# Kernel optimization log

Hardware: AMD Instinct MI355X
Metric: run time of the kernel (lower is better)

## Reference

```python
import jax, jax.numpy as jnp
import numpy as np

N_NODES = 50000
N_EDGES = 800000
D_IN = 128
D_OUT = 128


def setup_inputs() -> dict:
    key = jax.random.key(0)
    k1, k2, k3, k4, k5, k6 = jax.random.split(key, 6)
    curr_fea = jax.random.normal(k1, (N_NODES, D_IN), dtype=jnp.float32)
    edge_index = jax.random.randint(k2, (2, N_EDGES), 0, N_NODES, dtype=jnp.int64)
    s = 1.0 / np.sqrt(D_IN)
    W_self = jax.random.uniform(k3, (D_OUT, D_IN), jnp.float32, -s, s)
    b_self = jax.random.uniform(k4, (D_OUT,), jnp.float32, -s, s)
    W_neig = jax.random.uniform(k5, (D_OUT, D_IN), jnp.float32, -s, s)
    b_neig = jax.random.uniform(k6, (D_OUT,), jnp.float32, -s, s)
    return {"curr_fea": curr_fea, "edge_index": edge_index,
            "W_self": W_self, "b_self": b_self,
            "W_neig": W_neig, "b_neig": b_neig}


def reference(curr_fea, edge_index, W_self, b_self, W_neig, b_neig):
    num_nodes = curr_fea.shape[0]
    src, dst = edge_index[0], edge_index[1]
    # symmetrize: messages flow both directions
    src_all = jnp.concatenate([src, dst], axis=0)  # [2E]
    dst_all = jnp.concatenate([dst, src], axis=0)  # [2E]
    # gather neighbor features then scatter-add into destination nodes
    nei_sum = jax.ops.segment_sum(curr_fea[src_all], dst_all,
                                  num_segments=num_nodes)  # [N, d]
    out = (curr_fea @ W_self.T + b_self) + (nei_sum @ W_neig.T + b_neig)
    return out
```

## Files before the change

kernel.cpp:

```cpp
#include <hip/hip_runtime.h>

#define DD 128
#define BM 64
#define BK 32
#define BKN 64
#define NBMAX 1024
#define ECH 2048
#define CAP 2304
#define PADC 136

typedef __attribute__((ext_vector_type(8))) short bf16x8;
typedef __attribute__((ext_vector_type(4))) float f32x4;

__device__ __forceinline__ unsigned short f2b(float x) {
    unsigned u = __float_as_uint(x);
    u += 0x7fffu + ((u >> 16) & 1u);
    return (unsigned short)(u >> 16);
}
__device__ __forceinline__ float b2f_lo(unsigned v) { return __uint_as_float(v << 16); }
__device__ __forceinline__ float b2f_hi(unsigned v) { return __uint_as_float(v & 0xffff0000u); }
__device__ __forceinline__ float bf(unsigned short u) {
    return __uint_as_float((unsigned)u << 16);
}

__device__ __forceinline__ int detect_rf(const void* ei_raw, int E, int lane) {
    const unsigned long long* p = (const unsigned long long*)ei_raw;
    int n64 = E < 64 ? E : 64;
    bool big = (lane < n64) && (p[lane] >= (1ULL << 32));
    return (__ballot(big) == 0ULL) ? 1 : 0;
}

__global__ void detect_kernel(const unsigned long long* __restrict__ ei,
                              int n64, int* __restrict__ flag) {
    int i = threadIdx.x;
    bool big = (i < n64) && (ei[i] >= (1ULL << 32));
    unsigned long long b = __ballot(big);
    if (i == 0) *flag = (b == 0ULL) ? 1 : 0;
}

__global__ void cvt_all_kernel(const float* __restrict__ fea,
                               const float* __restrict__ Ws,
                               const float* __restrict__ Wn,
                               unsigned short* __restrict__ feaB,
                               unsigned short* __restrict__ Wcat, int n4) {
    int i = blockIdx.x * 256 + threadIdx.x;
    if (i < n4) {
        float4 v = reinterpret_cast<const float4*>(fea)[i];
        ushort4 o;
        o.x = f2b(v.x); o.y = f2b(v.y); o.z = f2b(v.z); o.w = f2b(v.w);
        reinterpret_cast<ushort4*>(feaB)[i] = o;
    } else if (i < n4 + 2 * DD * DD / 4) {
        int k4 = i - n4;
        int n = k4 >> 6;
        int kk = (k4 & 63) * 4;
        float4 v = (kk < DD) ? *reinterpret_cast<const float4*>(Ws + n * DD + kk)
                             : *reinterpret_cast<const float4*>(Wn + n * DD + kk - DD);
        ushort4 o;
        o.x = f2b(v.x); o.y = f2b(v.y); o.z = f2b(v.z); o.w = f2b(v.w);
        reinterpret_cast<ushort4*>(Wcat)[k4] = o;
    }
}

__global__ void cvt_fea_kernel(const float* __restrict__ in,
                               unsigned short* __restrict__ out, int n4) {
    int i = blockIdx.x * 256 + threadIdx.x;
    if (i >= n4) return;
    float4 v = reinterpret_cast<const float4*>(in)[i];
    ushort4 o;
    o.x = f2b(v.x); o.y = f2b(v.y); o.z = f2b(v.z); o.w = f2b(v.w);
    reinterpret_cast<ushort4*>(out)[i] = o;
}

__global__ void cvt_w_kernel(const float* __restrict__ Ws,
                             const float* __restrict__ Wn,
                             unsigned short* __restrict__ Wcat) {
    int i = blockIdx.x * 256 + threadIdx.x;
    int n = i >> 8, k = i & 255;
    float v = (k < DD) ? Ws[n * DD + k] : Wn[n * DD + (k - DD)];
    Wcat[i] = f2b(v);
}

__launch_bounds__(512)
__global__ void bin_kernel(const void* __restrict__ ei_raw, int E,
                           unsigned* __restrict__ region,
                           unsigned* __restrict__ gcur, int nbk) {
    __shared__ unsigned stage[2 * ECH];
    __shared__ unsigned cnt[NBMAX];
    __shared__ unsigned start[NBMAX];
    __shared__ unsigned cursor[NBMAX];
    __shared__ unsigned gbase[NBMAX];
    __shared__ unsigned scanT[512];

    const int t = threadIdx.x;
    const int lane = t & 63;
    const int rf = detect_rf(ei_raw, E, lane);

    for (int b = t; b < NBMAX; b += 512) { cnt[b] = 0; cursor[b] = 0; }
    __syncthreads();

    const int e0 = blockIdx.x * ECH;
    int es[4], ed[4];
#pragma unroll
    for (int j = 0; j < 4; ++j) {
        int e = e0 + j * 512 + t;
        if (e < E) {
            if (rf) {
                const long long* p = (const long long*)ei_raw;
                es[j] = (int)p[e]; ed[j] = (int)p[e + E];
            } else {
                const int* p = (const int*)ei_raw;
                es[j] = p[e]; ed[j] = p[e + E];
            }
            atomicAdd(&cnt[ed[j] >> 6], 1u);
            atomicAdd(&cnt[es[j] >> 6], 1u);
        } else {
            es[j] = -1; ed[j] = -1;
        }
    }
    __syncthreads();

    unsigned lv[2]; unsigned lsum = 0;
#pragma unroll
    for (int j = 0; j < 2; ++j) { lv[j] = cnt[t * 2 + j]; lsum += lv[j]; }
    scanT[t] = lsum; __syncthreads();
    for (int o = 1; o < 512; o <<= 1) {
        unsigned x = (t >= o) ? scanT[t - o] : 0;
        __syncthreads();
        scanT[t] += x;
        __syncthreads();
    }
    unsigned run = scanT[t] - lsum;
#pragma unroll
    for (int j = 0; j < 2; ++j) { start[t * 2 + j] = run; run += lv[j]; }
    __syncthreads();

#pragma unroll
    for (int j = 0; j < 4; ++j) {
        if (es[j] >= 0) {
            int s = es[j], d = ed[j];
            unsigned p0 = atomicAdd(&cursor[d >> 6], 1u);
            stage[start[d >> 6] + p0] = (unsigned)(d & 63) | ((unsigned)s << 6);
            unsigned p1 = atomicAdd(&cursor[s >> 6], 1u);
            stage[start[s >> 6] + p1] = (unsigned)(s & 63) | ((unsigned)d << 6);
        }
    }
    __syncthreads();

    for (int b = t; b < nbk; b += 512) {
        unsigned c = cnt[b];
        gbase[b] = c ? atomicAdd(&gcur[b], c) : 0;
    }
    __syncthreads();

    const int w = t >> 6;
    for (int b = w; b < nbk; b += 8) {
        unsigned c = cnt[b];
        if (!c) continue;
        unsigned gb = gbase[b], st = start[b];
        for (unsigned l2 = lane; l2 < c; l2 += 64) {
            unsigned idx = gb + l2;
            if (idx < CAP)
                region[(size_t)b * CAP + idx] = stage[st + l2];
        }
    }
}

__launch_bounds__(512)
__global__ void gather_gemm_kernel(const unsigned short* __restrict__ feaB,
                                   const unsigned short* __restrict__ Wcat,
                                   const unsigned* __restrict__ region,
                                   const unsigned* __restrict__ gcur,
                                   const float* __restrict__ bs,
                                   const float* __restrict__ bn,
                                   float* __restrict__ out, int M) {
    __shared__ unsigned srt[CAP];
    __shared__ unsigned short neiL[BKN][PADC];
    __shared__ unsigned c64[BKN];
    __shared__ unsigned p64[BKN + 1];
    __shared__ unsigned cur64[BKN];

    const int t = threadIdx.x, b = blockIdx.x;
    unsigned cnt = gcur[b];
    if (cnt > CAP) cnt = CAP;
    const unsigned* reg = region + (size_t)b * CAP;

    unsigned ent[5];
#pragma unroll
    for (int q = 0; q < 5; ++q) {
        unsigned i = (unsigned)t + (unsigned)q * 512u;
        ent[q] = (i < cnt) ? reg[i] : 0xFFFFFFFFu;
    }

    if (t < BKN) { c64[t] = 0; cur64[t] = 0; }
    __syncthreads();

#pragma unroll
    for (int q = 0; q < 5; ++q)
        if (ent[q] != 0xFFFFFFFFu) atomicAdd(&c64[ent[q] & 63u], 1u);
    __syncthreads();

    if (t == 0) {
        unsigned r = 0;
        for (int n = 0; n < BKN; ++n) { p64[n] = r; r += c64[n]; }
        p64[BKN] = r;
    }
    __syncthreads();

#pragma unroll
    for (int q = 0; q < 5; ++q) {
        if (ent[q] != 0xFFFFFFFFu) {
            unsigned e = ent[q];
            unsigned p = atomicAdd(&cur64[e & 63u], 1u);
            srt[p64[e & 63u] + p] = e >> 6;
        }
    }
    __syncthreads();

    const int w = t >> 6, lane = t & 63;
    const int half = lane >> 5, li = lane & 31;
    const unsigned short* bp = feaB + li * 4;

    for (int n = w; n < BKN; n += 8) {
        int g = b * BKN + n;
        unsigned p = p64[n];
        unsigned d = (g < M) ? c64[n] : 0;
        float a0 = 0.f, a1 = 0.f, a2 = 0.f, a3 = 0.f;
        unsigned j = 0;
        for (; j + 16 <= d; j += 16) {
            ushort4 v[8];
#pragma unroll
            for (int q = 0; q < 8; ++q) {
                unsigned s = srt[p + j + 2 * q + half];
                v[q] = *reinterpret_cast<const ushort4*>(bp + (size_t)s * DD);
            }
#pragma unroll
            for (int q = 0; q < 8; ++q) {
                a0 += bf(v[q].x); a1 += bf(v[q].y);
                a2 += bf(v[q].z); a3 += bf(v[q].w);
            }
        }
        for (; j + 2 <= d; j += 2) {
            unsigned s = srt[p + j + half];
            ushort4 v = *reinterpret_cast<const ushort4*>(bp + (size_t)s * DD);
            a0 += bf(v.x); a1 += bf(v.y); a2 += bf(v.z); a3 += bf(v.w);
        }
        if (j < d && half == 0) {
            unsigned s = srt[p + j];
            ushort4 v = *reinterpret_cast<const ushort4*>(bp + (size_t)s * DD);
            a0 += bf(v.x); a1 += bf(v.y); a2 += bf(v.z); a3 += bf(v.w);
        }
        a0 += __shfl_xor(a0, 32);
        a1 += __shfl_xor(a1, 32);
        a2 += __shfl_xor(a2, 32);
        a3 += __shfl_xor(a3, 32);
        if (half == 0) {
            ushort4 o;
            o.x = f2b(a0); o.y = f2b(a1); o.z = f2b(a2); o.w = f2b(a3);
            *reinterpret_cast<ushort4*>(&neiL[n][li * 4]) = o;
        }
    }
    __syncthreads();

    const int lr = lane & 15, ks = lane >> 4;
    const int rg = w & 3, cgr = w >> 2;
    const int row0 = b * BKN + rg * 16;
    const int rowl = rg * 16 + lr;
    const int rowg = row0 + lr;
    const int col0 = cgr * 64;

    f32x4 acc[4] = {};
#pragma unroll
    for (int kb = 0; kb < 256; kb += 32) {
        bf16x8 a;
        if (kb < DD) {
            if (rowg < M)
                a = *reinterpret_cast<const bf16x8*>(
                    feaB + (size_t)rowg * DD + kb + ks * 8);
            else
                a = bf16x8{0, 0, 0, 0, 0, 0, 0, 0};
        } else {
            a = *reinterpret_cast<const bf16x8*>(&neiL[rowl][(kb - DD) + ks * 8]);
        }
#pragma unroll
        for (int ci = 0; ci < 4; ++ci) {
            int nn = col0 + ci * 16 + lr;
            bf16x8 bb = *reinterpret_cast<const bf16x8*>(
                Wcat + (size_t)nn * 256 + kb + ks * 8);
            acc[ci] = __builtin_amdgcn_mfma_f32_16x16x32_bf16(a, bb, acc[ci], 0, 0, 0);
        }
    }

#pragma unroll
    for (int ci = 0; ci < 4; ++ci) {
        int colg = col0 + ci * 16 + lr;
        float bias = bs[colg] + bn[colg];
        int rbase = row0 + ks * 4;
#pragma unroll
        for (int i2 = 0; i2 < 4; ++i2) {
            int r2 = rbase + i2;
            if (r2 < M) out[(size_t)r2 * DD + colg] = acc[ci][i2] + bias;
        }
    }
}

__global__ void transpose_kernel(const float* __restrict__ Ws,
                                 const float* __restrict__ Wn,
                                 float* __restrict__ Wts,
                                 float* __restrict__ Wtn) {
    int idx = blockIdx.x * blockDim.x + threadIdx.x;
    int i = idx & (DD * DD - 1);
    int col = i >> 7;
    int k = i & (DD - 1);
    if (idx < DD * DD)          Wts[k * DD + col] = Ws[i];
    else if (idx < 2 * DD * DD) Wtn[k * DD + col] = Wn[i];
}

__global__ void hist_kernel(const void* __restrict__ ei_raw,
                            int* __restrict__ deg, int E,
                            const int* __restrict__ flag) {
    int e = blockIdx.x * 256 + threadIdx.x;
    if (e >= E) return;
    int s, d;
    if (*flag) {
        const long long* ei = (const long long*)ei_raw;
        s = (int)ei[e]; d = (int)ei[e + E];
    } else {
        const int* ei = (const int*)ei_raw;
        s = ei[e]; d = ei[e + E];
    }
    atomicAdd(&deg[s], 1);
    atomicAdd(&deg[d], 1);
}

__global__ void scan1_kernel(const int* __restrict__ deg, int* __restrict__ off,
                             int* __restrict__ bsum, int N) {
    __shared__ int sd[256];
    int base = blockIdx.x * 1024;
    int t = threadIdx.x;
    int v[4]; int s = 0;
#pragma unroll
    for (int j = 0; j < 4; ++j) {
        int idx = base + t * 4 + j;
        v[j] = (idx < N) ? deg[idx] : 0;
        s += v[j];
    }
    sd[t] = s; __syncthreads();
    for (int o = 1; o < 256; o <<= 1) {
        int x = (t >= o) ? sd[t - o] : 0;
        __syncthreads();
        sd[t] += x;
        __syncthreads();
    }
    int run = sd[t] - s;
    if (t == 255) bsum[blockIdx.x] = sd[255];
#pragma unroll
    for (int j = 0; j < 4; ++j) {
        int idx = base + t * 4 + j;
        if (idx < N) off[idx] = run;
        run += v[j];
    }
}

__global__ void scan2_kernel(int* __restrict__ bsum, int NB,
                             int* __restrict__ total) {
    __shared__ int sd[256];
    int t = threadIdx.x;
    int v = (t < NB) ? bsum[t] : 0;
    sd[t] = v; __syncthreads();
    for (int o = 1; o < 256; o <<= 1) {
        int x = (t >= o) ? sd[t - o] : 0;
        __syncthreads();
        sd[t] += x;
        __syncthreads();
    }
    if (t < NB) bsum[t] = sd[t] - v;
    if (t == 255) *total = sd[255];
}

__global__ void scan3_kernel(int* __restrict__ off, const int* __restrict__ bsum,
                             int N) {
    int i = blockIdx.x * blockDim.x + threadIdx.x;
    if (i < N) off[i] += bsum[i >> 10];
}

__global__ void fill_kernel(const void* __restrict__ ei_raw,
                            const int* __restrict__ off,
                            int* __restrict__ cursor, int* __restrict__ list,
                            int E, const int* __restrict__ flag) {
    int e = blockIdx.x * 256 + threadIdx.x;
    if (e >= E) return;
    int s, d;
    if (*flag) {
        const long long* ei = (const long long*)ei_raw;
        s = (int)ei[e]; d = (int)ei[e + E];
    } else {
        const int* ei = (const int*)ei_raw;
        s = ei[e]; d = ei[e + E];
    }
    int p0 = atomicAdd(&cursor[d], 1); list[off[d] + p0] = s;
    int p1 = atomicAdd(&cursor[s], 1); list[off[s] + p1] = d;
}

__launch_bounds__(256)
__global__ void gather_b_kernel(const unsigned short* __restrict__ feaB,
                                const int* __restrict__ off,
                                const int* __restrict__ list,
                                unsigned short* __restrict__ neiB, int N) {
    int w = (int)((blockIdx.x * 256 + threadIdx.x) >> 6);
    if (w >= N) return;
    int lane = threadIdx.x & 63;
    int start = off[w], end = off[w + 1];
    float ax = 0.f, ay = 0.f;
    const unsigned short* base = feaB + lane * 2;
    int j = start;
    for (; j + 4 <= end; j += 4) {
        int s0 = list[j], s1 = list[j + 1], s2 = list[j + 2], s3 = list[j + 3];
        unsigned a = *reinterpret_cast<const unsigned*>(base + (size_t)s0 * DD);
        unsigned b = *reinterpret_cast<const unsigned*>(base + (size_t)s1 * DD);
        unsigned c = *reinterpret_cast<const unsigned*>(base + (size_t)s2 * DD);
        unsigned d = *reinterpret_cast<const unsigned*>(base + (size_t)s3 * DD);
        ax += b2f_lo(a) + b2f_lo(b) + b2f_lo(c) + b2f_lo(d);
        ay += b2f_hi(a) + b2f_hi(b) + b2f_hi(c) + b2f_hi(d);
    }
    for (; j < end; ++j) {
        unsigned a = *reinterpret_cast<const unsigned*>(base + (size_t)list[j] * DD);
        ax += b2f_lo(a); ay += b2f_hi(a);
    }
    ushort2 o; o.x = f2b(ax); o.y = f2b(ay);
    *reinterpret_cast<ushort2*>(neiB + (size_t)w * DD + lane * 2) = o;
}

__launch_bounds__(256)
__global__ void gather_f32_kernel(const float* __restrict__ fea,
                                  const int* __restrict__ off,
                                  const int* __restrict__ list,
                                  float* __restrict__ nei, int N) {
    int w = (int)((blockIdx.x * 256 + threadIdx.x) >> 6);
    if (w >= N) return;
    int lane = threadIdx.x & 63;
    int start = off[w], end = off[w + 1];
    float2 acc = make_float2(0.f, 0.f);
    const float* base = fea + (size_t)lane * 2;
    int j = start;
    for (; j + 4 <= end; j += 4) {
        int s0 = list[j], s1 = list[j + 1], s2 = list[j + 2], s3 = list[j + 3];
        float2 a = *reinterpret_cast<const float2*>(base + (size_t)s0 * DD);
        float2 b = *reinterpret_cast<const float2*>(base + (size_t)s1 * DD);
        float2 c = *reinterpret_cast<const float2*>(base + (size_t)s2 * DD);
        float2 e = *reinterpret_cast<const float2*>(base + (size_t)s3 * DD);
        acc.x += a.x + b.x + c.x + e.x;
        acc.y += a.y + b.y + c.y + e.y;
    }
    for (; j < end; ++j) {
        float2 a = *reinterpret_cast<const float2*>(base + (size_t)list[j] * DD);
        acc.x += a.x; acc.y += a.y;
    }
    *reinterpret_cast<float2*>(nei + (size_t)w * DD + lane * 2) = acc;
}

__global__ void scatter_kernel(const float* __restrict__ fea,
                               const void* __restrict__ ei_raw,
                               float* __restrict__ nei,
                               int E, const int* __restrict__ flag) {
    long long r = (long long)blockIdx.x * 8 + (threadIdx.x >> 5);
    if (r >= 2LL * E) return;
    int lr = threadIdx.x & 31;
    int i = (int)(r < E ? r : r - E);
    int s, d;
    if (*flag) {
        const long long* ei = (const long long*)ei_raw;
        s = (int)ei[i]; d = (int)ei[i + E];
    } else {
        const int* ei = (const int*)ei_raw;
        s = ei[i]; d = ei[i + E];
    }
    if (r >= E) { int t = s; s = d; d = t; }
    const float4 v = *reinterpret_cast<const float4*>(fea + (size_t)s * DD + lr * 4);
    float* p = nei + (size_t)d * DD + lr * 4;
    unsafeAtomicAdd(p + 0, v.x);
    unsafeAtomicAdd(p + 1, v.y);
    unsafeAtomicAdd(p + 2, v.z);
    unsafeAtomicAdd(p + 3, v.w);
}

__launch_bounds__(256)
__global__ void gemm_mfma_kernel(const unsigned short* __restrict__ feaB,
                                 const unsigned short* __restrict__ neiB,
                                 const unsigned short* __restrict__ Wcat,
                                 const float* __restrict__ bs,
                                 const float* __restrict__ bn,
                                 float* __restrict__ out, int M) {
    const int w  = threadIdx.x >> 6;
    const int l  = threadIdx.x & 63;
    const int lr = l & 15;
    const int ks = l >> 4;
    const int row0 = blockIdx.x * 128 + w * 32;
    const int col0 = blockIdx.y * 64;

    f32x4 acc[2][4] = {};

#pragma unroll
    for (int kb = 0; kb < 256; kb += 32) {
        const unsigned short* A = (kb < DD) ? feaB : neiB;
        const int klocal = (kb < DD) ? kb : kb - DD;
        bf16x8 a[2];
#pragma unroll
        for (int ri = 0; ri < 2; ++ri) {
            int rowg = row0 + ri * 16 + lr;
            if (rowg < M)
                a[ri] = *reinterpret_cast<const bf16x8*>(
                    A + (size_t)rowg * DD + klocal + ks * 8);
            else
                a[ri] = bf16x8{0, 0, 0, 0, 0, 0, 0, 0};
        }
#pragma unroll
        for (int ci = 0; ci < 4; ++ci) {
            int n = col0 + ci * 16 + lr;
            bf16x8 b = *reinterpret_cast<const bf16x8*>(
                Wcat + (size_t)n * 256 + kb + ks * 8);
#pragma unroll
            for (int ri = 0; ri < 2; ++ri)
                acc[ri][ci] = __builtin_amdgcn_mfma_f32_16x16x32_bf16(
                    a[ri], b, acc[ri][ci], 0, 0, 0);
        }
    }

#pragma unroll
    for (int ci = 0; ci < 4; ++ci) {
        int colg = col0 + ci * 16 + lr;
        float bias = bs[colg] + bn[colg];
#pragma unroll
        for (int ri = 0; ri < 2; ++ri) {
            int rbase = row0 + ri * 16 + ks * 4;
#pragma unroll
            for (int i = 0; i < 4; ++i) {
                int rowg = rbase + i;
                if (rowg < M)
                    out[(size_t)rowg * DD + colg] = acc[ri][ci][i] + bias;
            }
        }
    }
}

__launch_bounds__(256)
__global__ void gemm_kernel(const float* __restrict__ fea,
                            const float* __restrict__ nei,
                            const float* __restrict__ Wts,
                            const float* __restrict__ Wtn,
                            const float* __restrict__ bs,
                            const float* __restrict__ bn,
                            float* __restrict__ out, int M) {
    __shared__ float Fs[BM][BK + 4];
    __shared__ float Ns[BM][BK + 4];
    __shared__ float WsT[BK][DD];
    __shared__ float WnT[BK][DD];

    const int t = threadIdx.x;
    const int cg = t & 31;
    const int rg = t >> 5;
    const int row0 = blockIdx.x * BM;

    float4 acc[8];
#pragma unroll
    for (int r = 0; r < 8; ++r) acc[r] = make_float4(0.f, 0.f, 0.f, 0.f);

    for (int kb = 0; kb < DD; kb += BK) {
#pragma unroll
        for (int j = 0; j < 2; ++j) {
            int idx = t + j * 256;
            int row = idx >> 3;
            int seg = idx & 7;
            int grow = row0 + row;
            float4 fv = make_float4(0.f, 0.f, 0.f, 0.f);
            float4 nv = make_float4(0.f, 0.f, 0.f, 0.f);
            if (grow < M) {
                fv = *reinterpret_cast<const float4*>(fea + (size_t)grow * DD + kb + seg * 4);
                nv = *reinterpret_cast<const float4*>(nei + (size_t)grow * DD + kb + seg * 4);
            }
            *reinterpret_cast<float4*>(&Fs[row][seg * 4]) = fv;
            *reinterpret_cast<float4*>(&Ns[row][seg * 4]) = nv;
        }
#pragma unroll
        for (int j = 0; j < 4; ++j) {
            int idx = t + j * 256;
            int kk = idx >> 5;
            int seg = idx & 31;
            *reinterpret_cast<float4*>(&WsT[kk][seg * 4]) =
                *reinterpret_cast<const float4*>(Wts + (size_t)(kb + kk) * DD + seg * 4);
            *reinterpret_cast<float4*>(&WnT[kk][seg * 4]) =
                *reinterpret_cast<const float4*>(Wtn + (size_t)(kb + kk) * DD + seg * 4);
        }
        __syncthreads();

#pragma unroll
        for (int kk = 0; kk < BK; ++kk) {
            float4 wsv = *reinterpret_cast<const float4*>(&WsT[kk][cg * 4]);
            float4 wnv = *reinterpret_cast<const float4*>(&WnT[kk][cg * 4]);
#pragma unroll
            for (int r = 0; r < 8; ++r) {
                float a = Fs[rg * 8 + r][kk];
                float b = Ns[rg * 8 + r][kk];
                acc[r].x += a * wsv.x + b * wnv.x;
                acc[r].y += a * wsv.y + b * wnv.y;
                acc[r].z += a * wsv.z + b * wnv.z;
                acc[r].w += a * wsv.w + b * wnv.w;
            }
        }
        __syncthreads();
    }

    float4 bsv = *reinterpret_cast<const float4*>(bs + cg * 4);
    float4 bnv = *reinterpret_cast<const float4*>(bn + cg * 4);
    float4 bias = make_float4(bsv.x + bnv.x, bsv.y + bnv.y, bsv.z + bnv.z, bsv.w + bnv.w);
#pragma unroll
    for (int r = 0; r < 8; ++r) {
        int grow = row0 + rg * 8 + r;
        if (grow < M) {
            float4 o = make_float4(acc[r].x + bias.x, acc[r].y + bias.y,
                                   acc[r].z + bias.z, acc[r].w + bias.w);
            *reinterpret_cast<float4*>(out + (size_t)grow * DD + cg * 4) = o;
        }
    }
}

extern "C" void kernel_launch(void* const* d_in, const int* in_sizes, int n_in,
                              void* d_out, int out_size, void* d_ws, size_t ws_size,
                              hipStream_t stream) {
    const float* fea = (const float*)d_in[0];
    const void*  ei  = d_in[1];
    const float* Ws  = (const float*)d_in[2];
    const float* bsv = (const float*)d_in[3];
    const float* Wn  = (const float*)d_in[4];
    const float* bnv = (const float*)d_in[5];

    const int M = in_sizes[0] / DD;
    const int E = in_sizes[1] / 2;
    float* out = (float*)d_out;
    char* ws = (char*)d_ws;
    int* flag = (int*)ws;

    const int NBK = (M + BKN - 1) / BKN;
    const size_t csr_bytes = (size_t)M * 8 + (size_t)(M + 1) * 4 + 4096
                           + (size_t)2 * E * 4;

    size_t o1 = 256;
    unsigned short* Wcat = (unsigned short*)(ws + o1); o1 += (size_t)DD * 256 * 2;
    unsigned short* feaB = (unsigned short*)(ws + o1); o1 += (size_t)M * DD * 2;
    unsigned* gcur  = (unsigned*)(ws + o1);            o1 += 4096;
    unsigned* region = (unsigned*)(ws + o1);           o1 += (size_t)NBK * CAP * 4;
    size_t need1 = o1;

    size_t o2 = 256 + (size_t)DD * 256 * 2 + (size_t)M * DD * 2;
    unsigned short* neiB2 = (unsigned short*)(ws + o2);
    size_t o2b = o2 + (size_t)M * DD * 2;
    size_t need2 = o2b + csr_bytes;

    size_t o3 = 256;
    float* Wts = (float*)(ws + o3); o3 += (size_t)DD * DD * 4;
    float* Wtn = (float*)(ws + o3); o3 += (size_t)DD * DD * 4;
    size_t need3 = o3 + csr_bytes;

    const int NB = (M + 1023) / 1024;
    const int eb = (E + 255) / 256;
    const int n4 = M * DD / 4;

    if (ws_size >= need1 && NBK <= NBMAX) {
        hipMemsetAsync(gcur, 0, 4096, stream);
        int cvtb = (n4 + 2 * DD * DD / 4 + 255) / 256;
        cvt_all_kernel<<<cvtb, 256, 0, stream>>>(fea, Ws, Wn, feaB, Wcat, n4);
        int abks = (E + ECH - 1) / ECH;
        bin_kernel<<<abks, 512, 0, stream>>>(ei, E, region, gcur, NBK);
        gather_gemm_kernel<<<NBK, 512, 0, stream>>>(feaB, Wcat, region, gcur,
                                                    bsv, bnv, out, M);
    } else if (ws_size >= need2) {
        int* deg    = (int*)(ws + o2b);
        int* cursor = deg + M;
        int* off    = cursor + M;
        int* bsum   = off + (M + 1);
        int* list   = bsum + 1024;

        detect_kernel<<<1, 64, 0, stream>>>((const unsigned long long*)ei,
                                            E < 64 ? E : 64, flag);
        cvt_fea_kernel<<<(n4 + 255) / 256, 256, 0, stream>>>(fea, feaB, n4);
        cvt_w_kernel<<<(DD * 256 + 255) / 256, 256, 0, stream>>>(Ws, Wn, Wcat);
        hipMemsetAsync(deg, 0, (size_t)2 * M * 4, stream);
        hist_kernel<<<eb, 256, 0, stream>>>(ei, deg, E, flag);
        scan1_kernel<<<NB, 256, 0, stream>>>(deg, off, bsum, M);
        scan2_kernel<<<1, 256, 0, stream>>>(bsum, NB, &off[M]);
        scan3_kernel<<<(M + 255) / 256, 256, 0, stream>>>(off, bsum, M);
        fill_kernel<<<eb, 256, 0, stream>>>(ei, off, cursor, list, E, flag);
        gather_b_kernel<<<(M + 3) / 4, 256, 0, stream>>>(feaB, off, list, neiB2, M);
        dim3 g((M + 127) / 128, 2);
        gemm_mfma_kernel<<<g, 256, 0, stream>>>(feaB, neiB2, Wcat, bsv, bnv, out, M);
    } else if (ws_size >= need3) {
        int* deg    = (int*)(ws + o3);
        int* cursor = deg + M;
        int* off    = cursor + M;
        int* bsum   = off + (M + 1);
        int* list   = bsum + 1024;
        float* nei = out;

        detect_kernel<<<1, 64, 0, stream>>>((const unsigned long long*)ei,
                                            E < 64 ? E : 64, flag);
        transpose_kernel<<<(2 * DD * DD + 255) / 256, 256, 0, stream>>>(Ws, Wn, Wts, Wtn);
        hipMemsetAsync(deg, 0, (size_t)2 * M * 4, stream);
        hist_kernel<<<eb, 256, 0, stream>>>(ei, deg, E, flag);
        scan1_kernel<<<NB, 256, 0, stream>>>(deg, off, bsum, M);
        scan2_kernel<<<1, 256, 0, stream>>>(bsum, NB, &off[M]);
        scan3_kernel<<<(M + 255) / 256, 256, 0, stream>>>(off, bsum, M);
        fill_kernel<<<eb, 256, 0, stream>>>(ei, off, cursor, list, E, flag);
        gather_f32_kernel<<<(M + 3) / 4, 256, 0, stream>>>(fea, off, list, nei, M);
        gemm_kernel<<<(M + BM - 1) / BM, 256, 0, stream>>>(fea, nei, Wts, Wtn,
                                                           bsv, bnv, out, M);
    } else {
        float* nei = out;
        detect_kernel<<<1, 64, 0, stream>>>((const unsigned long long*)ei,
                                            E < 64 ? E : 64, flag);
        transpose_kernel<<<(2 * DD * DD + 255) / 256, 256, 0, stream>>>(Ws, Wn, Wts, Wtn);
        hipMemsetAsync(nei, 0, (size_t)M * DD * 4, stream);
        long long rows = 2LL * E;
        int sblocks = (int)((rows + 7) / 8);
        scatter_kernel<<<sblocks, 256, 0, stream>>>(fea, ei, nei, E, flag);
        gemm_kernel<<<(M + BM - 1) / BM, 256, 0, stream>>>(fea, nei, Wts, Wtn,
                                                           bsv, bnv, out, M);
    }
}
```

Before: 206.2 us.

## Split each 64-node bucket across two 256-thread blocks and use wave scan

The fused gather+GEMM kernel now launches two 256-thread blocks per 64-node bucket. Each block handles 32 destination nodes, which doubles the grid to improve occupancy and load balance. Both blocks still read and sort the whole bucket's edge list, so that binning work is duplicated. The serial single-thread prefix sum over 64 counts is replaced by a wavefront shuffle scan.

```diff
diff --git a/kernel.cpp b/kernel.cpp
--- a/kernel.cpp
+++ b/kernel.cpp
@@ -4,6 +4,7 @@
 #define BM 64
 #define BK 32
 #define BKN 64
+#define NPB 32
 #define NBMAX 1024
 #define ECH 2048
 #define CAP 2304
@@ -165,29 +166,30 @@
     }
 }
 
-__launch_bounds__(512)
-__global__ void gather_gemm_kernel(const unsigned short* __restrict__ feaB,
-                                   const unsigned short* __restrict__ Wcat,
-                                   const unsigned* __restrict__ region,
-                                   const unsigned* __restrict__ gcur,
-                                   const float* __restrict__ bs,
-                                   const float* __restrict__ bn,
-                                   float* __restrict__ out, int M) {
+__launch_bounds__(256)
+__global__ void gather_gemm2_kernel(const unsigned short* __restrict__ feaB,
+                                    const unsigned short* __restrict__ Wcat,
+                                    const unsigned* __restrict__ region,
+                                    const unsigned* __restrict__ gcur,
+                                    const float* __restrict__ bs,
+                                    const float* __restrict__ bn,
+                                    float* __restrict__ out, int M) {
     __shared__ unsigned srt[CAP];
-    __shared__ unsigned short neiL[BKN][PADC];
+    __shared__ unsigned short neiL[NPB][PADC];
     __shared__ unsigned c64[BKN];
-    __shared__ unsigned p64[BKN + 1];
+    __shared__ unsigned p64[BKN];
     __shared__ unsigned cur64[BKN];
 
-    const int t = threadIdx.x, b = blockIdx.x;
+    const int t = threadIdx.x;
+    const int b2 = blockIdx.x, b = b2 >> 1, h = b2 & 1;
     unsigned cnt = gcur[b];
     if (cnt > CAP) cnt = CAP;
     const unsigned* reg = region + (size_t)b * CAP;
 
-    unsigned ent[5];
-#pragma unroll
-    for (int q = 0; q < 5; ++q) {
-        unsigned i = (unsigned)t + (unsigned)q * 512u;
+    unsigned ent[9];
+#pragma unroll
+    for (int q = 0; q < 9; ++q) {
+        unsigned i = (unsigned)t + (unsigned)q * 256u;
         ent[q] = (i < cnt) ? reg[i] : 0xFFFFFFFFu;
     }
 
@@ -195,19 +197,24 @@
     __syncthreads();
 
 #pragma unroll
-    for (int q = 0; q < 5; ++q)
+    for (int q = 0; q < 9; ++q)
         if (ent[q] != 0xFFFFFFFFu) atomicAdd(&c64[ent[q] & 63u], 1u);
     __syncthreads();
 
-    if (t == 0) {
-        unsigned r = 0;
-        for (int n = 0; n < BKN; ++n) { p64[n] = r; r += c64[n]; }
-        p64[BKN] = r;
-    }
-    __syncthreads();
-
-#pragma unroll
-    for (int q = 0; q < 5; ++q) {
+    if (t < 64) {
+        unsigned v = c64[t];
+        unsigned sc = v;
+#pragma unroll
+        for (int o = 1; o < 64; o <<= 1) {
+            unsigned x = __shfl_up(sc, o, 64);
+            if (t >= o) sc += x;
+        }
+        p64[t] = sc - v;
+    }
+    __syncthreads();
+
+#pragma unroll
+    for (int q = 0; q < 9; ++q) {
         if (ent[q] != 0xFFFFFFFFu) {
             unsigned e = ent[q];
             unsigned p = atomicAdd(&cur64[e & 63u], 1u);
@@ -220,7 +227,7 @@
     const int half = lane >> 5, li = lane & 31;
     const unsigned short* bp = feaB + li * 4;
 
-    for (int n = w; n < BKN; n += 8) {
+    for (int n = h * NPB + w; n < h * NPB + NPB; n += 4) {
         int g = b * BKN + n;
         unsigned p = p64[n];
         unsigned d = (g < M) ? c64[n] : 0;
@@ -256,14 +263,14 @@
         if (half == 0) {
             ushort4 o;
             o.x = f2b(a0); o.y = f2b(a1); o.z = f2b(a2); o.w = f2b(a3);
-            *reinterpret_cast<ushort4*>(&neiL[n][li * 4]) = o;
+            *reinterpret_cast<ushort4*>(&neiL[n - h * NPB][li * 4]) = o;
         }
     }
     __syncthreads();
 
     const int lr = lane & 15, ks = lane >> 4;
-    const int rg = w & 3, cgr = w >> 2;
-    const int row0 = b * BKN + rg * 16;
+    const int rg = w & 1, cgr = w >> 1;
+    const int row0 = b2 * NPB + rg * 16;
     const int rowl = rg * 16 + lr;
     const int rowg = row0 + lr;
     const int col0 = cgr * 64;
@@ -670,8 +677,8 @@
         cvt_all_kernel<<<cvtb, 256, 0, stream>>>(fea, Ws, Wn, feaB, Wcat, n4);
         int abks = (E + ECH - 1) / ECH;
         bin_kernel<<<abks, 512, 0, stream>>>(ei, E, region, gcur, NBK);
-        gather_gemm_kernel<<<NBK, 512, 0, stream>>>(feaB, Wcat, region, gcur,
-                                                    bsv, bnv, out, M);
+        gather_gemm2_kernel<<<2 * NBK, 256, 0, stream>>>(feaB, Wcat, region, gcur,
+                                                         bsv, bnv, out, M);
     } else if (ws_size >= need2) {
         int* deg    = (int*)(ws + o2b);
         int* cursor = deg + M;
```

Result: faster. 199.6 us (-3.2%).
